# Optimization experiments

Measured on AMD Instinct MI355X. Metric: run time of the kernel, lower is better.

## Reference

```python
import math
import jax, jax.numpy as jnp
import numpy as np

B, N, D, H, NI, NL, NS, MID = 32, 2048, 256, 8, 64, 3, 32, 3


def _ln(x, g, b, eps=1e-5):
    m = jnp.mean(x, axis=-1, keepdims=True)
    v = jnp.mean((x - m) ** 2, axis=-1, keepdims=True)
    return (x - m) * jax.lax.rsqrt(v + eps) * g + b


def _mab(Q, K, mask, Wq, bq, Wk, bk, Wv, bv, Wo, bo, g0, b0, g1, b1):
    # torch's split(dim_split,2)+cat(...,0) == reshape to (B, n, H, dh)
    dh = D // H
    q = (Q @ Wq + bq).reshape(Q.shape[0], Q.shape[1], H, dh)
    k = (K @ Wk + bk).reshape(K.shape[0], K.shape[1], H, dh)
    v = (K @ Wv + bv).reshape(K.shape[0], K.shape[1], H, dh)
    A = jnp.einsum('bqhd,bkhd->bhqk', q, k) / math.sqrt(D)  # note: sqrt(dim_V), faithful
    A = jnp.where(mask[:, None, None, :] == 0, -1e4, A)
    A = jax.nn.softmax(A, axis=-1)
    o = q + jnp.einsum('bhqk,bkhd->bqhd', A, v)
    O = o.reshape(Q.shape[0], Q.shape[1], D)
    O = _ln(O, g0, b0)
    O = O + jax.nn.relu(O @ Wo + bo)
    return _ln(O, g1, b1)


def _forward(x_values, y_target, point_mask, proj_W, proj_b, isab_I,
             isab_Wq, isab_bq, isab_Wk, isab_bk, isab_Wv, isab_bv,
             isab_Wo, isab_bo, isab_g0, isab_b0, isab_g1, isab_b1,
             pma_S, pma_Wq, pma_bq, pma_Wk, pma_bk, pma_Wv, pma_bv,
             pma_Wo, pma_bo, pma_g0, pma_b0, pma_g1, pma_b1):
    # input_dim == max_input_dim, so the zero-padded feature build is a concat
    feats = jnp.concatenate([x_values, y_target[..., None]], axis=-1)  # (B, N, MID+1)
    x = jax.nn.gelu(feats @ proj_W + proj_b, approximate=False)
    ones_mask = jnp.ones((x.shape[0], NI), jnp.float32)
    stk = (isab_Wq, isab_bq, isab_Wk, isab_bk, isab_Wv, isab_bv,
           isab_Wo, isab_bo, isab_g0, isab_b0, isab_g1, isab_b1)
    for l in range(NL):
        I = jnp.broadcast_to(isab_I[l][None], (x.shape[0], NI, D))
        h = _mab(I, x, point_mask, *[a[l, 0] for a in stk])   # mab0: inducing pts attend to X
        x = _mab(x, h, ones_mask, *[a[l, 1] for a in stk])    # mab1: X attends to H (all valid)
    S = jnp.broadcast_to(pma_S[None], (x.shape[0], NS, D))
    return _mab(S, x, point_mask, pma_Wq, pma_bq, pma_Wk, pma_bk, pma_Wv,
                pma_bv, pma_Wo, pma_bo, pma_g0, pma_b0, pma_g1, pma_b1)


def setup_inputs():
    key = jax.random.key(0)
    ks = iter(jax.random.split(key, 40))
    def nrm(shape, s=0.05):
        return jax.random.normal(next(ks), shape, dtype=jnp.float32) * s
    z = lambda shape: jnp.zeros(shape, jnp.float32)
    o = lambda shape: jnp.ones(shape, jnp.float32)
    return {
        'x_values': jax.random.normal(next(ks), (B, N, MID), jnp.float32),
        'y_target': jax.random.normal(next(ks), (B, N), jnp.float32),
        'point_mask': jax.random.randint(next(ks), (B, N), 0, 2).astype(jnp.float32),
        'proj_W': nrm((MID + 1, D)), 'proj_b': z((D,)),
        'isab_I': nrm((NL, NI, D), 0.1),
        'isab_Wq': nrm((NL, 2, D, D)), 'isab_bq': z((NL, 2, D)),
        'isab_Wk': nrm((NL, 2, D, D)), 'isab_bk': z((NL, 2, D)),
        'isab_Wv': nrm((NL, 2, D, D)), 'isab_bv': z((NL, 2, D)),
        'isab_Wo': nrm((NL, 2, D, D)), 'isab_bo': z((NL, 2, D)),
        'isab_g0': o((NL, 2, D)), 'isab_b0': z((NL, 2, D)),
        'isab_g1': o((NL, 2, D)), 'isab_b1': z((NL, 2, D)),
        'pma_S': nrm((NS, D), 0.1),
        'pma_Wq': nrm((D, D)), 'pma_bq': z((D,)),
        'pma_Wk': nrm((D, D)), 'pma_bk': z((D,)),
        'pma_Wv': nrm((D, D)), 'pma_bv': z((D,)),
        'pma_Wo': nrm((D, D)), 'pma_bo': z((D,)),
        'pma_g0': o((D,)), 'pma_b0': z((D,)),
        'pma_g1': o((D,)), 'pma_b1': z((D,)),
    }


def reference(x_values, y_target, point_mask, proj_W, proj_b, isab_I,
              isab_Wq, isab_bq, isab_Wk, isab_bk, isab_Wv, isab_bv,
              isab_Wo, isab_bo, isab_g0, isab_b0, isab_g1, isab_b1,
              pma_S, pma_Wq, pma_bq, pma_Wk, pma_bk, pma_Wv, pma_bv,
              pma_Wo, pma_bo, pma_g0, pma_b0, pma_g1, pma_b1):
    return _forward(x_values, y_target, point_mask, proj_W, proj_b, isab_I,
                    isab_Wq, isab_bq, isab_Wk, isab_bk, isab_Wv, isab_bv,
                    isab_Wo, isab_bo, isab_g0, isab_b0, isab_g1, isab_b1,
                    pma_S, pma_Wq, pma_bq, pma_Wk, pma_bk, pma_Wv, pma_bv,
                    pma_Wo, pma_bo, pma_g0, pma_b0, pma_g1, pma_b1)
```

## Files before the change

kernel.cpp:

```cpp
#include <hip/hip_runtime.h>
#include <hip/hip_bf16.h>


typedef __attribute__((ext_vector_type(8))) short short8;
typedef __attribute__((ext_vector_type(4))) float f32x4;
typedef __attribute__((ext_vector_type(4))) ushort ushort4v;

__device__ __forceinline__ ushort f2bf(float f) {
  uint u = __builtin_bit_cast(uint, f);
  u += 0x7fffu + ((u >> 16) & 1u);
  return (ushort)(u >> 16);
}
__device__ __forceinline__ float bf2f(ushort h) {
  uint u = (uint)h << 16;
  return __builtin_bit_cast(float, u);
}

__global__ __launch_bounds__(256) void prep_weights(
    const float* __restrict__ Wq, const float* __restrict__ Wk,
    const float* __restrict__ Wv, const float* __restrict__ Wo,
    const float* __restrict__ pWq, const float* __restrict__ pWk,
    const float* __restrict__ pWv, const float* __restrict__ pWo,
    ushort* __restrict__ wt)
{
  __shared__ float tile[64][65];
  const int m = blockIdx.y;
  const int t = blockIdx.x;
  const int tr = (t >> 2) * 64;
  const int tc = (t & 3) * 64;
  const float* src;
  if (m < 24) {
    int l = m >> 3, s = (m >> 2) & 1, w = m & 3;
    const float* base = (w == 0) ? Wq : (w == 1) ? Wk : (w == 2) ? Wv : Wo;
    src = base + (size_t)(l * 2 + s) * 65536;
  } else {
    int w = m & 3;
    src = (w == 0) ? pWq : (w == 1) ? pWk : (w == 2) ? pWv : pWo;
  }
  const int tid = threadIdx.x;
  const int cn = tid & 63;
  const int rk = tid >> 6;
#pragma unroll
  for (int j = 0; j < 16; ++j) {
    int kl = rk + j * 4;
    tile[kl][cn] = src[(size_t)(tr + kl) * 256 + tc + cn];
  }
  __syncthreads();
  ushort* dst = wt + (size_t)m * 65536;
#pragma unroll
  for (int j = 0; j < 16; ++j) {
    int nl = rk + j * 4;
    dst[(size_t)(tc + nl) * 256 + tr + cn] = f2bf(tile[cn][nl]);
  }
}

__global__ __launch_bounds__(256) void proj_gelu(
    const float* __restrict__ xv, const float* __restrict__ yt,
    const float* __restrict__ pW, const float* __restrict__ pb,
    ushort* __restrict__ xb)
{
  const int d = threadIdx.x;
  const int row0 = blockIdx.x * 8;
  const float w0 = pW[d], w1 = pW[256 + d], w2 = pW[512 + d], w3 = pW[768 + d];
  const float bz = pb[d];
#pragma unroll
  for (int rr = 0; rr < 8; ++rr) {
    int row = row0 + rr;
    float f0 = xv[(size_t)row * 3 + 0];
    float f1 = xv[(size_t)row * 3 + 1];
    float f2 = xv[(size_t)row * 3 + 2];
    float f3 = yt[row];
    float a = bz + f0 * w0 + f1 * w1 + f2 * w2 + f3 * w3;
    float g = 0.5f * a * (1.f + erff(a * 0.70710678118654752f));
    xb[(size_t)row * 256 + d] = f2bf(g);
  }
}

__global__ __launch_bounds__(256) void gemm_q(
    const float* __restrict__ iI, const float* __restrict__ pS,
    const ushort* __restrict__ wt, const float* __restrict__ ibq,
    const float* __restrict__ pbq, ushort* __restrict__ q_all)
{
  const int bq = blockIdx.x;
  const float* A; const ushort* Wt; const float* bias; ushort* out; int M;
  if (bq < 3) { A = iI + bq * 16384; Wt = wt + (size_t)(bq * 8) * 65536; bias = ibq + bq * 512; out = q_all + bq * 16384; M = 64; }
  else        { A = pS; Wt = wt + (size_t)24 * 65536; bias = pbq; out = q_all + 49152; M = 32; }
  const int tid = threadIdx.x;
  const int wave = tid >> 6, lane = tid & 63;
  const int l15 = lane & 15, l4 = lane >> 4, koff = l4 * 8;
  f32x4 acc[4][4];
#pragma unroll
  for (int i = 0; i < 4; ++i)
#pragma unroll
    for (int j = 0; j < 4; ++j) acc[i][j] = (f32x4)0.f;
#pragma unroll
  for (int ks = 0; ks < 8; ++ks) {
    short8 af[4];
#pragma unroll
    for (int mf = 0; mf < 4; ++mf) {
      if (mf * 16 < M) {
        const float* ap = A + (size_t)(mf * 16 + l15) * 256 + ks * 32 + koff;
        float4 f0 = *(const float4*)ap;
        float4 f1 = *(const float4*)(ap + 4);
        short8 sv;
        sv[0] = (short)f2bf(f0.x); sv[1] = (short)f2bf(f0.y);
        sv[2] = (short)f2bf(f0.z); sv[3] = (short)f2bf(f0.w);
        sv[4] = (short)f2bf(f1.x); sv[5] = (short)f2bf(f1.y);
        sv[6] = (short)f2bf(f1.z); sv[7] = (short)f2bf(f1.w);
        af[mf] = sv;
      } else af[mf] = (short8)0;
    }
#pragma unroll
    for (int nf = 0; nf < 4; ++nf) {
      short8 bf = *(const short8*)(Wt + (size_t)(wave * 64 + nf * 16 + l15) * 256 + ks * 32 + koff);
#pragma unroll
      for (int mf = 0; mf < 4; ++mf)
        acc[mf][nf] = __builtin_amdgcn_mfma_f32_16x16x32_bf16(af[mf], bf, acc[mf][nf], 0, 0, 0);
    }
  }
#pragma unroll
  for (int mf = 0; mf < 4; ++mf) {
    if (mf * 16 >= M) continue;
#pragma unroll
    for (int nf = 0; nf < 4; ++nf) {
      int col = wave * 64 + nf * 16 + l15;
      float bcol = bias[col];
#pragma unroll
      for (int r = 0; r < 4; ++r)
        out[(size_t)(mf * 16 + l4 * 4 + r) * 256 + col] = f2bf(acc[mf][nf][r] + bcol);
    }
  }
}

template <int EPI, bool OUTF32, int COLS>
__global__ __launch_bounds__(COLS * 2, (COLS == 128) ? 4 : 2) void gemm_bp(
    const ushort* __restrict__ A,
    const ushort* __restrict__ Wt0, const ushort* __restrict__ Wt1, const ushort* __restrict__ Wt2,
    const float* __restrict__ b0, const float* __restrict__ b1, const float* __restrict__ b2,
    void* __restrict__ o0, void* __restrict__ o1, void* __restrict__ o2,
    const float* __restrict__ lng, const float* __restrict__ lnb,
    int ny, int nyz)
{
  constexpr int WC = COLS / 64;
  constexpr int PS = COLS * 64;
  constexpr int ROWB = COLS * 2;
  __shared__ __align__(16) char Bs[4 * PS];
  __shared__ float redbuf[(EPI == 3) ? 1280 : 4];
  const int bid = blockIdx.x;
  const int rest = bid >> 3;
  const int yz = rest % nyz;
  const int bx = ((rest / nyz) << 3) | (bid & 7);
  const int y = yz % ny;
  const int z = yz / ny;
  const ushort* Wt = (z == 0) ? Wt0 : ((z == 1) ? Wt1 : Wt2);
  const float* bias = (z == 0) ? b0 : ((z == 1) ? b1 : b2);
  void* outp = (z == 0) ? o0 : ((z == 1) ? o1 : o2);
  const int pcol = y * COLS;

  const int tid = threadIdx.x;
  const int wave = tid >> 6, lane = tid & 63;
  const int wc = wave % WC, wr = wave / WC;
  const int l15 = lane & 15, l4 = lane >> 4;
  const int row0 = bx * 128;
  const int sn = tid >> 1, sseg = tid & 1;

  f32x4 acc[4][4];
#pragma unroll
  for (int i = 0; i < 4; ++i)
#pragma unroll
    for (int j = 0; j < 4; ++j) acc[i][j] = (f32x4)0.f;

#pragma unroll
  for (int half = 0; half < 2; ++half) {
    if (half) __syncthreads();
    {
      const ushort* src = Wt + (size_t)(pcol + sn) * 256 + half * 128 + sseg * 64;
#pragma unroll
      for (int c = 0; c < 8; ++c) {
        uint4 w = *(const uint4*)(src + c * 8);
        int plane = sseg * 2 + (c >> 2);
        char* dst = Bs + plane * PS + sn * 64 + (((c & 3) * 16) ^ (((sn >> 1) & 3) << 4));
        *(uint4*)dst = w;
      }
    }
    __syncthreads();
#pragma unroll
    for (int ks = 0; ks < 4; ++ks) {
      short8 af[4];
#pragma unroll
      for (int mfa = 0; mfa < 4; ++mfa)
        af[mfa] = *(const short8*)(A + (size_t)(row0 + wr * 64 + mfa * 16 + l15) * 256 + half * 128 + ks * 32 + l4 * 8);
#pragma unroll
      for (int nfb = 0; nfb < 4; ++nfb) {
        int n = wc * 64 + nfb * 16 + l15;
        short8 bf = *(const short8*)(Bs + ks * PS + n * 64 + ((l4 * 16) ^ (((n >> 1) & 3) << 4)));
#pragma unroll
        for (int mfa = 0; mfa < 4; ++mfa)
          acc[mfa][nfb] = __builtin_amdgcn_mfma_f32_16x16x32_bf16(bf, af[mfa], acc[mfa][nfb], 0, 0, 0);
      }
    }
  }

  if constexpr (EPI == 0) {
    __syncthreads();
#pragma unroll
    for (int nfb = 0; nfb < 4; ++nfb) {
      f32x4 bv = *(const f32x4*)(bias + pcol + wc * 64 + nfb * 16 + l4 * 4);
      int colb = wc * 128 + nfb * 32 + l4 * 8;
#pragma unroll
      for (int mfa = 0; mfa < 4; ++mfa) {
        int row = wr * 64 + mfa * 16 + l15;
        ushort4v pk;
#pragma unroll
        for (int i = 0; i < 4; ++i) pk[i] = f2bf(acc[mfa][nfb][i] + bv[i]);
        *(ushort4v*)(Bs + row * ROWB + (colb ^ ((row & 7) << 4))) = pk;
      }
    }
    __syncthreads();
    const int srow = tid >> 2, seg = tid & 3;
#pragma unroll
    for (int rr = 0; rr < 2; ++rr) {
      int row = srow + rr * 64;
      int x = (row & 7) << 4;
      ushort* gdst = (ushort*)outp + (size_t)(row0 + row) * 256 + pcol;
#pragma unroll
      for (int it = 0; it < 4; ++it) {
        int colb = seg * 16 + it * 64;
        uint4 v = *(const uint4*)(Bs + row * ROWB + (colb ^ x));
        *(uint4*)(gdst + colb / 2) = v;
      }
    }
  } else {
    float* red1 = redbuf;
    float* red2 = redbuf + 512;
    float* mv_ = redbuf + 1024;
    float* rv_ = redbuf + 1152;
    float s1[4] = {0.f, 0.f, 0.f, 0.f}, s2[4] = {0.f, 0.f, 0.f, 0.f};
#pragma unroll
    for (int nfb = 0; nfb < 4; ++nfb) {
      int col0 = wc * 64 + nfb * 16 + l4 * 4;
      f32x4 bv = *(const f32x4*)(bias + col0);
#pragma unroll
      for (int mfa = 0; mfa < 4; ++mfa) {
        size_t row = (size_t)row0 + wr * 64 + mfa * 16 + l15;
        ushort4v rz = *(const ushort4v*)(A + row * 256 + col0);
#pragma unroll
        for (int i = 0; i < 4; ++i) {
          float zz = bf2f(rz[i]) + fmaxf(acc[mfa][nfb][i] + bv[i], 0.f);
          acc[mfa][nfb][i] = zz;
          s1[mfa] += zz;
          s2[mfa] += zz * zz;
        }
      }
    }
#pragma unroll
    for (int mfa = 0; mfa < 4; ++mfa) {
      s1[mfa] += __shfl_xor(s1[mfa], 16); s1[mfa] += __shfl_xor(s1[mfa], 32);
      s2[mfa] += __shfl_xor(s2[mfa], 16); s2[mfa] += __shfl_xor(s2[mfa], 32);
    }
    if (l4 == 0) {
#pragma unroll
      for (int mfa = 0; mfa < 4; ++mfa) {
        red1[wc * 128 + wr * 64 + mfa * 16 + l15] = s1[mfa];
        red2[wc * 128 + wr * 64 + mfa * 16 + l15] = s2[mfa];
      }
    }
    __syncthreads();
    if (tid < 128) {
      float m1 = red1[tid] + red1[128 + tid] + red1[256 + tid] + red1[384 + tid];
      float m2 = red2[tid] + red2[128 + tid] + red2[256 + tid] + red2[384 + tid];
      float mean = m1 * 0.00390625f;
      float var = m2 * 0.00390625f - mean * mean;
      mv_[tid] = mean;
      rv_[tid] = rsqrtf(var + 1e-5f);
    }
    __syncthreads();
#pragma unroll
    for (int nfb = 0; nfb < 4; ++nfb) {
      int col0 = wc * 64 + nfb * 16 + l4 * 4;
      f32x4 gg = *(const f32x4*)(lng + col0);
      f32x4 bb = *(const f32x4*)(lnb + col0);
      int colb = col0 * 2;
#pragma unroll
      for (int mfa = 0; mfa < 4; ++mfa) {
        int lr = wr * 64 + mfa * 16 + l15;
        float mean = mv_[lr], rs = rv_[lr];
        if constexpr (OUTF32) {
          f32x4 w;
#pragma unroll
          for (int i = 0; i < 4; ++i) w[i] = (acc[mfa][nfb][i] - mean) * rs * gg[i] + bb[i];
          *(f32x4*)((float*)outp + ((size_t)row0 + lr) * 256 + col0) = w;
        } else {
          ushort4v pk;
#pragma unroll
          for (int i = 0; i < 4; ++i) pk[i] = f2bf((acc[mfa][nfb][i] - mean) * rs * gg[i] + bb[i]);
          *(ushort4v*)(Bs + lr * ROWB + (colb ^ ((lr & 7) << 4))) = pk;
        }
      }
    }
    if constexpr (!OUTF32) {
      __syncthreads();
      const int srow = tid >> 2, seg = tid & 3;
      int x = (srow & 7) << 4;
      ushort* gdst = (ushort*)outp + (size_t)(row0 + srow) * 256;
#pragma unroll
      for (int it = 0; it < 8; ++it) {
        int colb = seg * 16 + it * 64;
        uint4 v = *(const uint4*)(Bs + srow * ROWB + (colb ^ x));
        *(uint4*)(gdst + colb / 2) = v;
      }
    }
  }
}

template <int MF>
__global__ __launch_bounds__(512) void attn_big(
    const ushort* __restrict__ qb, const ushort* __restrict__ kb,
    const ushort* __restrict__ vb, const float* __restrict__ mask,
    ushort* __restrict__ O)
{
  __shared__ __align__(16) ushort Ps[8][64][72];
  __shared__ __align__(16) ushort Vt[8][32][72];
  const int h = blockIdx.x, b = blockIdx.y;
  const int tid = threadIdx.x;
  const int w = tid >> 6, lane = tid & 63;
  const int l15 = lane & 15, l4 = lane >> 4;
  const int koff = l4 * 8;
  const int kvbase = b * 2048;

  short8 qf[MF];
#pragma unroll
  for (int mf = 0; mf < MF; ++mf)
    qf[mf] = *(const short8*)(qb + (size_t)(mf * 16 + l15) * 256 + h * 32 + koff);

  f32x4 Oa[MF][2];
  float Mr[MF][4], Lr[MF][4];
#pragma unroll
  for (int mf = 0; mf < MF; ++mf) {
    Oa[mf][0] = (f32x4)0.f; Oa[mf][1] = (f32x4)0.f;
#pragma unroll
    for (int r = 0; r < 4; ++r) { Mr[mf][r] = -1e30f; Lr[mf][r] = 0.f; }
  }

  for (int c = 0; c < 4; ++c) {
    const int kc = w * 256 + c * 64;
    f32x4 S[MF][4];
#pragma unroll
    for (int nf = 0; nf < 4; ++nf) {
      short8 kf = *(const short8*)(kb + (size_t)(kvbase + kc + nf * 16 + l15) * 256 + h * 32 + koff);
#pragma unroll
      for (int mf = 0; mf < MF; ++mf)
        S[mf][nf] = __builtin_amdgcn_mfma_f32_16x16x32_bf16(qf[mf], kf, (f32x4)0.f, 0, 0, 0);
    }
    float mv[4];
#pragma unroll
    for (int nf = 0; nf < 4; ++nf)
      mv[nf] = mask[(size_t)b * 2048 + kc + nf * 16 + l15];
#pragma unroll
    for (int mf = 0; mf < MF; ++mf)
#pragma unroll
      for (int nf = 0; nf < 4; ++nf)
#pragma unroll
        for (int r = 0; r < 4; ++r) {
          float s = S[mf][nf][r] * 0.0625f;
          S[mf][nf][r] = (mv[nf] != 0.f) ? s : -1e4f;
        }
#pragma unroll
    for (int mf = 0; mf < MF; ++mf)
#pragma unroll
      for (int r = 0; r < 4; ++r) {
        float pm = fmaxf(fmaxf(S[mf][0][r], S[mf][1][r]), fmaxf(S[mf][2][r], S[mf][3][r]));
        pm = fmaxf(pm, __shfl_xor(pm, 1));
        pm = fmaxf(pm, __shfl_xor(pm, 2));
        pm = fmaxf(pm, __shfl_xor(pm, 4));
        pm = fmaxf(pm, __shfl_xor(pm, 8));
        float Mnew = fmaxf(Mr[mf][r], pm);
        float corr = __expf(Mr[mf][r] - Mnew);
        Mr[mf][r] = Mnew;
        float rs = 0.f;
#pragma unroll
        for (int nf = 0; nf < 4; ++nf) {
          float p = __expf(S[mf][nf][r] - Mnew);
          S[mf][nf][r] = p;
          rs += p;
        }
        rs += __shfl_xor(rs, 1);
        rs += __shfl_xor(rs, 2);
        rs += __shfl_xor(rs, 4);
        rs += __shfl_xor(rs, 8);
        Lr[mf][r] = Lr[mf][r] * corr + rs;
        Oa[mf][0][r] *= corr;
        Oa[mf][1][r] *= corr;
      }
#pragma unroll
    for (int dblk = 0; dblk < 4; ++dblk) {
      short8 vv = *(const short8*)(vb + (size_t)(kvbase + kc + lane) * 256 + h * 32 + dblk * 8);
#pragma unroll
      for (int j = 0; j < 8; ++j) Vt[w][dblk * 8 + j][lane] = (ushort)vv[j];
    }
#pragma unroll
    for (int mf = 0; mf < MF; ++mf)
#pragma unroll
      for (int nf = 0; nf < 4; ++nf)
#pragma unroll
        for (int r = 0; r < 4; ++r)
          Ps[w][mf * 16 + l4 * 4 + r][nf * 16 + l15] = f2bf(S[mf][nf][r]);
#pragma unroll
    for (int ks = 0; ks < 2; ++ks) {
      short8 pf[MF];
#pragma unroll
      for (int mf = 0; mf < MF; ++mf)
        pf[mf] = *(const short8*)&Ps[w][mf * 16 + l15][ks * 32 + koff];
#pragma unroll
      for (int nf2 = 0; nf2 < 2; ++nf2) {
        short8 vf = *(const short8*)&Vt[w][nf2 * 16 + l15][ks * 32 + koff];
#pragma unroll
        for (int mf = 0; mf < MF; ++mf)
          Oa[mf][nf2] = __builtin_amdgcn_mfma_f32_16x16x32_bf16(pf[mf], vf, Oa[mf][nf2], 0, 0, 0);
      }
    }
  }

  __syncthreads();
  float* Mw = (float*)&Ps[0][0][0];
  float* Lw = Mw + 512;
  float* Ow = Lw + 512;
#pragma unroll
  for (int mf = 0; mf < MF; ++mf)
#pragma unroll
    for (int r = 0; r < 4; ++r) {
      int row = mf * 16 + l4 * 4 + r;
      if (l15 == 0) { Mw[w * 64 + row] = Mr[mf][r]; Lw[w * 64 + row] = Lr[mf][r]; }
#pragma unroll
      for (int nf2 = 0; nf2 < 2; ++nf2)
        Ow[(w * 64 + row) * 33 + nf2 * 16 + l15] = Oa[mf][nf2][r];
    }
  __syncthreads();
  const int NQ = MF * 16;
  int row = tid >> 3, dg = tid & 7;
  if (row < NQ) {
    float mm = -1e30f;
#pragma unroll
    for (int s = 0; s < 8; ++s) mm = fmaxf(mm, Mw[s * 64 + row]);
    float den = 0.f, es[8];
#pragma unroll
    for (int s = 0; s < 8; ++s) {
      es[s] = __expf(Mw[s * 64 + row] - mm);
      den += Lw[s * 64 + row] * es[s];
    }
    float invden = 1.f / den;
    ushort4v pk;
#pragma unroll
    for (int i = 0; i < 4; ++i) {
      int d = dg * 4 + i;
      float num = 0.f;
#pragma unroll
      for (int s = 0; s < 8; ++s) num += Ow[(s * 64 + row) * 33 + d] * es[s];
      float qv = bf2f(qb[(size_t)row * 256 + h * 32 + d]);
      pk[i] = f2bf(qv + num * invden);
    }
    *(ushort4v*)(O + (size_t)(b * NQ + row) * 256 + h * 32 + dg * 4) = pk;
  }
}

__global__ __launch_bounds__(512, 4) void mab1_fused(
    const ushort* __restrict__ xb, const ushort* __restrict__ wq,
    const float* __restrict__ bq,
    const ushort* __restrict__ kb, const ushort* __restrict__ vb,
    const ushort* __restrict__ wo, const float* __restrict__ bo,
    const float* __restrict__ g0, const float* __restrict__ b0v,
    const float* __restrict__ g1, const float* __restrict__ b1v,
    ushort* __restrict__ outb)
{
  __shared__ __align__(16) ushort Qs[8][64][40];
  __shared__ __align__(16) ushort Psh[8][16][40];
  __shared__ __align__(16) ushort Vth[8][32][40];
  __shared__ float red1[8][64], red2[8][64], mv_[64], rv_[64];
  ushort* o_s = &Qs[0][0][0];
  constexpr int OS = 264;

  const int qt = blockIdx.x, b = blockIdx.y;
  const int tid = threadIdx.x;
  const int w = tid >> 6, lane = tid & 63;
  const int l15 = lane & 15, l4 = lane >> 4;
  const int koff = l4 * 8;
  const size_t row0 = (size_t)b * 2048 + qt * 64;
  const int kvbase = b * 64;
  const int h = w;

  short8 kf[4];
#pragma unroll
  for (int nf = 0; nf < 4; ++nf)
    kf[nf] = *(const short8*)(kb + (size_t)(kvbase + nf * 16 + l15) * 256 + h * 32 + koff);
  const int key = lane & 31, dh2 = lane >> 5;
  short8 vvB0, vvB1;
  {
    const ushort* vsrcA = vb + (size_t)(kvbase + key) * 256 + h * 32 + dh2 * 16;
    const ushort* vsrcB = vb + (size_t)(kvbase + 32 + key) * 256 + h * 32 + dh2 * 16;
    short8 vvA0 = *(const short8*)vsrcA;
    short8 vvA1 = *(const short8*)(vsrcA + 8);
    vvB0 = *(const short8*)vsrcB;
    vvB1 = *(const short8*)(vsrcB + 8);
#pragma unroll
    for (int j = 0; j < 8; ++j) Vth[w][dh2 * 16 + j][key] = (ushort)vvA0[j];
#pragma unroll
    for (int j = 0; j < 8; ++j) Vth[w][dh2 * 16 + 8 + j][key] = (ushort)vvA1[j];
  }

  {
    f32x4 qa[4][2];
#pragma unroll
    for (int i = 0; i < 4; ++i) { qa[i][0] = (f32x4)0.f; qa[i][1] = (f32x4)0.f; }
#pragma unroll
    for (int ks = 0; ks < 8; ++ks) {
      short8 af[4];
#pragma unroll
      for (int mfa = 0; mfa < 4; ++mfa)
        af[mfa] = *(const short8*)(xb + (row0 + mfa * 16 + l15) * 256 + ks * 32 + koff);
#pragma unroll
      for (int nfb = 0; nfb < 2; ++nfb) {
        int n = w * 32 + nfb * 16 + l15;
        short8 bf = *(const short8*)(wq + (size_t)n * 256 + ks * 32 + koff);
#pragma unroll
        for (int mfa = 0; mfa < 4; ++mfa)
          qa[mfa][nfb] = __builtin_amdgcn_mfma_f32_16x16x32_bf16(bf, af[mfa], qa[mfa][nfb], 0, 0, 0);
      }
    }
#pragma unroll
    for (int nfb = 0; nfb < 2; ++nfb) {
      f32x4 bv = *(const f32x4*)(bq + w * 32 + nfb * 16 + l4 * 4);
#pragma unroll
      for (int mfa = 0; mfa < 4; ++mfa) {
        ushort4v pk;
#pragma unroll
        for (int i = 0; i < 4; ++i) pk[i] = f2bf(qa[mfa][nfb][i] + bv[i]);
        *(ushort4v*)&Qs[w][mfa * 16 + l15][nfb * 16 + l4 * 4] = pk;
      }
    }
  }

  short8 qf[4];
#pragma unroll
  for (int mf = 0; mf < 4; ++mf)
    qf[mf] = *(const short8*)&Qs[w][mf * 16 + l15][koff];

  f32x4 S[4][4];
#pragma unroll
  for (int nf = 0; nf < 4; ++nf) {
#pragma unroll
    for (int mf = 0; mf < 4; ++mf)
      S[mf][nf] = __builtin_amdgcn_mfma_f32_16x16x32_bf16(qf[mf], kf[nf], (f32x4)0.f, 0, 0, 0);
  }
  float Lr[4][4];
#pragma unroll
  for (int mf = 0; mf < 4; ++mf)
#pragma unroll
    for (int r = 0; r < 4; ++r) {
      float pm = fmaxf(fmaxf(S[mf][0][r], S[mf][1][r]), fmaxf(S[mf][2][r], S[mf][3][r])) * 0.0625f;
      pm = fmaxf(pm, __shfl_xor(pm, 1));
      pm = fmaxf(pm, __shfl_xor(pm, 2));
      pm = fmaxf(pm, __shfl_xor(pm, 4));
      pm = fmaxf(pm, __shfl_xor(pm, 8));
      float rs = 0.f;
#pragma unroll
      for (int nf = 0; nf < 4; ++nf) {
        float p = __expf(S[mf][nf][r] * 0.0625f - pm);
        S[mf][nf][r] = p;
        rs += p;
      }
      rs += __shfl_xor(rs, 1);
      rs += __shfl_xor(rs, 2);
      rs += __shfl_xor(rs, 4);
      rs += __shfl_xor(rs, 8);
      Lr[mf][r] = rs;
    }

  f32x4 Oa[4][2];
#pragma unroll
  for (int mf = 0; mf < 4; ++mf) { Oa[mf][0] = (f32x4)0.f; Oa[mf][1] = (f32x4)0.f; }
#pragma unroll
  for (int mf = 0; mf < 4; ++mf) {
#pragma unroll
    for (int nf = 0; nf < 2; ++nf)
#pragma unroll
      for (int r = 0; r < 4; ++r)
        Psh[w][l4 * 4 + r][nf * 16 + l15] = f2bf(S[mf][nf][r]);
    short8 pf = *(const short8*)&Psh[w][l15][koff];
#pragma unroll
    for (int nf2 = 0; nf2 < 2; ++nf2) {
      short8 vf = *(const short8*)&Vth[w][nf2 * 16 + l15][koff];
      Oa[mf][nf2] = __builtin_amdgcn_mfma_f32_16x16x32_bf16(pf, vf, Oa[mf][nf2], 0, 0, 0);
    }
  }
#pragma unroll
  for (int j = 0; j < 8; ++j) Vth[w][dh2 * 16 + j][key] = (ushort)vvB0[j];
#pragma unroll
  for (int j = 0; j < 8; ++j) Vth[w][dh2 * 16 + 8 + j][key] = (ushort)vvB1[j];
#pragma unroll
  for (int mf = 0; mf < 4; ++mf) {
#pragma unroll
    for (int nf = 0; nf < 2; ++nf)
#pragma unroll
      for (int r = 0; r < 4; ++r)
        Psh[w][l4 * 4 + r][nf * 16 + l15] = f2bf(S[mf][nf + 2][r]);
    short8 pf = *(const short8*)&Psh[w][l15][koff];
#pragma unroll
    for (int nf2 = 0; nf2 < 2; ++nf2) {
      short8 vf = *(const short8*)&Vth[w][nf2 * 16 + l15][koff];
      Oa[mf][nf2] = __builtin_amdgcn_mfma_f32_16x16x32_bf16(pf, vf, Oa[mf][nf2], 0, 0, 0);
    }
  }

  {
    float s1[4][4], s2[4][4];
#pragma unroll
    for (int mf = 0; mf < 4; ++mf)
#pragma unroll
      for (int r = 0; r < 4; ++r) {
        float invL = 1.f / Lr[mf][r];
        s1[mf][r] = 0.f; s2[mf][r] = 0.f;
#pragma unroll
        for (int nf2 = 0; nf2 < 2; ++nf2) {
          float qv = bf2f(Qs[w][mf * 16 + l4 * 4 + r][nf2 * 16 + l15]);
          float z = qv + Oa[mf][nf2][r] * invL;
          Oa[mf][nf2][r] = z;
          s1[mf][r] += z;
          s2[mf][r] += z * z;
        }
#pragma unroll
        for (int off = 1; off < 16; off <<= 1) {
          s1[mf][r] += __shfl_xor(s1[mf][r], off);
          s2[mf][r] += __shfl_xor(s2[mf][r], off);
        }
        if (l15 == 0) {
          int row = mf * 16 + l4 * 4 + r;
          red1[w][row] = s1[mf][r];
          red2[w][row] = s2[mf][r];
        }
      }
  }
  __syncthreads();
  if (tid < 64) {
    float m1 = 0.f, m2 = 0.f;
#pragma unroll
    for (int s = 0; s < 8; ++s) { m1 += red1[s][tid]; m2 += red2[s][tid]; }
    float mean = m1 * 0.00390625f;
    float var = m2 * 0.00390625f - mean * mean;
    mv_[tid] = mean;
    rv_[tid] = rsqrtf(var + 1e-5f);
  }
  __syncthreads();
#pragma unroll
  for (int nf2 = 0; nf2 < 2; ++nf2) {
    int col = h * 32 + nf2 * 16 + l15;
    float gc = g0[col], bc = b0v[col];
#pragma unroll
    for (int mf = 0; mf < 4; ++mf)
#pragma unroll
      for (int r = 0; r < 4; ++r) {
        int row = mf * 16 + l4 * 4 + r;
        float v = (Oa[mf][nf2][r] - mv_[row]) * rv_[row] * gc + bc;
        o_s[row * OS + col] = f2bf(v);
      }
  }
  __syncthreads();

  f32x4 oa[4][2];
#pragma unroll
  for (int i = 0; i < 4; ++i) { oa[i][0] = (f32x4)0.f; oa[i][1] = (f32x4)0.f; }
#pragma unroll
  for (int ks = 0; ks < 8; ++ks) {
    short8 af[4];
#pragma unroll
    for (int mfa = 0; mfa < 4; ++mfa)
      af[mfa] = *(const short8*)&o_s[(mfa * 16 + l15) * OS + ks * 32 + koff];
#pragma unroll
    for (int nfb = 0; nfb < 2; ++nfb) {
      int n = w * 32 + nfb * 16 + l15;
      short8 bf = *(const short8*)(wo + (size_t)n * 256 + ks * 32 + koff);
#pragma unroll
      for (int mfa = 0; mfa < 4; ++mfa)
        oa[mfa][nfb] = __builtin_amdgcn_mfma_f32_16x16x32_bf16(bf, af[mfa], oa[mfa][nfb], 0, 0, 0);
    }
  }
  float t1[4] = {0.f, 0.f, 0.f, 0.f}, t2[4] = {0.f, 0.f, 0.f, 0.f};
#pragma unroll
  for (int nfb = 0; nfb < 2; ++nfb) {
    int col0 = w * 32 + nfb * 16 + l4 * 4;
    f32x4 bv = *(const f32x4*)(bo + col0);
#pragma unroll
    for (int mfa = 0; mfa < 4; ++mfa) {
      int row = mfa * 16 + l15;
      ushort4v rz = *(const ushort4v*)&o_s[row * OS + col0];
#pragma unroll
      for (int i = 0; i < 4; ++i) {
        float zz = bf2f(rz[i]) + fmaxf(oa[mfa][nfb][i] + bv[i], 0.f);
        oa[mfa][nfb][i] = zz;
        t1[mfa] += zz;
        t2[mfa] += zz * zz;
      }
    }
  }
#pragma unroll
  for (int mfa = 0; mfa < 4; ++mfa) {
    t1[mfa] += __shfl_xor(t1[mfa], 16); t1[mfa] += __shfl_xor(t1[mfa], 32);
    t2[mfa] += __shfl_xor(t2[mfa], 16); t2[mfa] += __shfl_xor(t2[mfa], 32);
  }
  if (l4 == 0) {
#pragma unroll
    for (int mfa = 0; mfa < 4; ++mfa) {
      red1[w][mfa * 16 + l15] = t1[mfa];
      red2[w][mfa * 16 + l15] = t2[mfa];
    }
  }
  __syncthreads();
  if (tid < 64) {
    float m1 = 0.f, m2 = 0.f;
#pragma unroll
    for (int s = 0; s < 8; ++s) { m1 += red1[s][tid]; m2 += red2[s][tid]; }
    float mean = m1 * 0.00390625f;
    float var = m2 * 0.00390625f - mean * mean;
    mv_[tid] = mean;
    rv_[tid] = rsqrtf(var + 1e-5f);
  }
  __syncthreads();
#pragma unroll
  for (int nfb = 0; nfb < 2; ++nfb) {
    int col0 = w * 32 + nfb * 16 + l4 * 4;
    f32x4 gg = *(const f32x4*)(g1 + col0);
    f32x4 bb = *(const f32x4*)(b1v + col0);
#pragma unroll
    for (int mfa = 0; mfa < 4; ++mfa) {
      int row = mfa * 16 + l15;
      ushort4v pk;
#pragma unroll
      for (int i = 0; i < 4; ++i)
        pk[i] = f2bf((oa[mfa][nfb][i] - mv_[row]) * rv_[row] * gg[i] + bb[i]);
      *(ushort4v*)&o_s[row * OS + col0] = pk;
    }
  }
  __syncthreads();
  {
    const int r_ = tid >> 3, sg = tid & 7;
    ushort* gdst = outb + (row0 + r_) * 256 + sg * 32;
    const ushort* src = &o_s[r_ * OS + sg * 32];
#pragma unroll
    for (int it = 0; it < 4; ++it) {
      uint4 v = *(const uint4*)(src + it * 8);
      *(uint4*)(gdst + it * 8) = v;
    }
  }
}

__global__ __launch_bounds__(256) void ln4(
    const ushort* __restrict__ in, ushort* __restrict__ out,
    const float* __restrict__ g, const float* __restrict__ bb)
{
  const int w = threadIdx.x >> 6, lane = threadIdx.x & 63;
  const size_t row = (size_t)blockIdx.x * 4 + w;
  ushort4v u = *(const ushort4v*)(in + row * 256 + lane * 4);
  float v[4];
#pragma unroll
  for (int i = 0; i < 4; ++i) v[i] = bf2f(u[i]);
  float s1 = v[0] + v[1] + v[2] + v[3];
  float s2 = v[0] * v[0] + v[1] * v[1] + v[2] * v[2] + v[3] * v[3];
#pragma unroll
  for (int off = 1; off < 64; off <<= 1) {
    s1 += __shfl_xor(s1, off);
    s2 += __shfl_xor(s2, off);
  }
  float mean = s1 * 0.00390625f;
  float var = s2 * 0.00390625f - mean * mean;
  float rs = rsqrtf(var + 1e-5f);
  f32x4 gg = *(const f32x4*)(g + lane * 4);
  f32x4 bv = *(const f32x4*)(bb + lane * 4);
  ushort4v p;
#pragma unroll
  for (int i = 0; i < 4; ++i) p[i] = f2bf((v[i] - mean) * rs * gg[i] + bv[i]);
  *(ushort4v*)(out + row * 256 + lane * 4) = p;
}

extern "C" void kernel_launch(void* const* d_in, const int* in_sizes, int n_in,
                              void* d_out, int out_size, void* d_ws, size_t ws_size,
                              hipStream_t stream) {
  const float* xv = (const float*)d_in[0];
  const float* yt = (const float*)d_in[1];
  const float* pmask = (const float*)d_in[2];
  const float* prW = (const float*)d_in[3];
  const float* prb = (const float*)d_in[4];
  const float* iI = (const float*)d_in[5];
  const float* iWq = (const float*)d_in[6];
  const float* ibq = (const float*)d_in[7];
  const float* iWk = (const float*)d_in[8];
  const float* ibk = (const float*)d_in[9];
  const float* iWv = (const float*)d_in[10];
  const float* ibv = (const float*)d_in[11];
  const float* iWo = (const float*)d_in[12];
  const float* ibo = (const float*)d_in[13];
  const float* ig0 = (const float*)d_in[14];
  const float* ib0 = (const float*)d_in[15];
  const float* ig1 = (const float*)d_in[16];
  const float* ib1 = (const float*)d_in[17];
  const float* pS = (const float*)d_in[18];
  const float* pWq = (const float*)d_in[19];
  const float* pbq = (const float*)d_in[20];
  const float* pWk = (const float*)d_in[21];
  const float* pbk = (const float*)d_in[22];
  const float* pWv = (const float*)d_in[23];
  const float* pbv = (const float*)d_in[24];
  const float* pWo = (const float*)d_in[25];
  const float* pbo = (const float*)d_in[26];
  const float* pg0 = (const float*)d_in[27];
  const float* pb0 = (const float*)d_in[28];
  const float* pg1 = (const float*)d_in[29];
  const float* pb1 = (const float*)d_in[30];

  char* ws = (char*)d_ws;
  if (ws_size < 172621824u) return;
  ushort* xb = (ushort*)(ws + 0);
  ushort* ob = (ushort*)(ws + 33554432);
  ushort* hb = (ushort*)(ws + 67108864);
  ushort* kbw = (ushort*)(ws + 101711872);
  ushort* vbw = (ushort*)(ws + 135266304);
  ushort* wt = (ushort*)(ws + 168820736);
  ushort* q_all = (ushort*)(ws + 172490752);

  prep_weights<<<dim3(16, 28), 256, 0, stream>>>(iWq, iWk, iWv, iWo, pWq, pWk, pWv, pWo, wt);
  proj_gelu<<<8192, 256, 0, stream>>>(xv, yt, prW, prb, xb);
  gemm_q<<<4, 256, 0, stream>>>(iI, pS, wt, ibq, pbq, q_all);

  for (int l = 0; l < 3; ++l) {
    const int s0 = l * 2, s1 = l * 2 + 1;
    const ushort* wk = wt + (size_t)(l * 8 + 1) * 65536;
    const ushort* wv = wt + (size_t)(l * 8 + 2) * 65536;
    const ushort* wo0 = wt + (size_t)(l * 8 + 3) * 65536;
    const ushort* wq1 = wt + (size_t)(l * 8 + 4) * 65536;
    const ushort* wk1 = wt + (size_t)(l * 8 + 5) * 65536;
    const ushort* wv1 = wt + (size_t)(l * 8 + 6) * 65536;
    const ushort* wo1 = wt + (size_t)(l * 8 + 7) * 65536;
    gemm_bp<0, false, 128><<<2048, 256, 0, stream>>>(
        xb, wk, wv, wv, ibk + s0 * 256, ibv + s0 * 256, ibv + s0 * 256,
        kbw, vbw, vbw, nullptr, nullptr, 2, 4);
    attn_big<4><<<dim3(8, 32), 512, 0, stream>>>(q_all + l * 16384, kbw, vbw, pmask, ob);
    ln4<<<512, 256, 0, stream>>>(ob, ob, ig0 + s0 * 256, ib0 + s0 * 256);
    gemm_bp<3, false, 256><<<16, 512, 0, stream>>>(
        ob, wo0, wo0, wo0, ibo + s0 * 256, ibo + s0 * 256, ibo + s0 * 256,
        hb, hb, hb, ig1 + s0 * 256, ib1 + s0 * 256, 1, 1);
    gemm_bp<0, false, 128><<<64, 256, 0, stream>>>(
        hb, wk1, wv1, wv1, ibk + s1 * 256, ibv + s1 * 256, ibv + s1 * 256,
        kbw, vbw, vbw, nullptr, nullptr, 2, 4);
    mab1_fused<<<dim3(32, 32), 512, 0, stream>>>(
        xb, wq1, ibq + s1 * 256, kbw, vbw, wo1, ibo + s1 * 256,
        ig0 + s1 * 256, ib0 + s1 * 256, ig1 + s1 * 256, ib1 + s1 * 256, xb);
  }
  gemm_bp<0, false, 128><<<2048, 256, 0, stream>>>(
      xb, wt + (size_t)25 * 65536, wt + (size_t)26 * 65536, wt + (size_t)26 * 65536,
      pbk, pbv, pbv, kbw, vbw, vbw, nullptr, nullptr, 2, 4);
  attn_big<2><<<dim3(8, 32), 512, 0, stream>>>(q_all + 49152, kbw, vbw, pmask, ob);
  ln4<<<256, 256, 0, stream>>>(ob, ob, pg0, pb0);
  gemm_bp<3, true, 256><<<8, 512, 0, stream>>>(
      ob, wt + (size_t)27 * 65536, wt + (size_t)27 * 65536, wt + (size_t)27 * 65536,
      pbo, pbo, pbo, d_out, d_out, d_out, pg1, pb1, 1, 1);
}
```

Baseline: 799.5 us.

## Fuse K/V projection of X into the inducing-point attention kernel

The separate gemm_bp launch that projected all 65536 points to K and V is removed. The attention kernel, now with a (batch, head) grid, computes each head's 32-column slice of K and V on the fly from the bf16 X tile with MFMAs and stages the results in shared memory. This removes the global write and re-read of K/V, which are large (B*N*D in bf16, written then read back), and one kernel launch per layer. In exchange each block rereads the full 256-wide X rows once per head, so X traffic goes up eightfold (mostly from L2). It also adds projection compute inside the attention kernel, plus extra shared memory and registers.

```diff
diff --git a/kernel.cpp b/kernel.cpp
--- a/kernel.cpp
+++ b/kernel.cpp
@@ -314,14 +314,16 @@
 }
 
 template <int MF>
-__global__ __launch_bounds__(512) void attn_big(
-    const ushort* __restrict__ qb, const ushort* __restrict__ kb,
-    const ushort* __restrict__ vb, const float* __restrict__ mask,
-    ushort* __restrict__ O)
+__global__ __launch_bounds__(512) void attn_fused(
+    const ushort* __restrict__ qb, const ushort* __restrict__ xbuf,
+    const ushort* __restrict__ wk, const float* __restrict__ bk,
+    const ushort* __restrict__ wv, const float* __restrict__ bv,
+    const float* __restrict__ mask, ushort* __restrict__ O)
 {
   __shared__ __align__(16) ushort Ps[8][64][72];
   __shared__ __align__(16) ushort Vt[8][32][72];
-  const int h = blockIdx.x, b = blockIdx.y;
+  __shared__ __align__(16) ushort Kc[8][64][40];
+  const int b = blockIdx.x, h = blockIdx.y;
   const int tid = threadIdx.x;
   const int w = tid >> 6, lane = tid & 63;
   const int l15 = lane & 15, l4 = lane >> 4;
@@ -333,6 +335,13 @@
   for (int mf = 0; mf < MF; ++mf)
     qf[mf] = *(const short8*)(qb + (size_t)(mf * 16 + l15) * 256 + h * 32 + koff);
 
+  f32x4 bkv[2], bvv[2];
+#pragma unroll
+  for (int nfb = 0; nfb < 2; ++nfb) {
+    bkv[nfb] = *(const f32x4*)(bk + h * 32 + nfb * 16 + l4 * 4);
+    bvv[nfb] = *(const f32x4*)(bv + h * 32 + nfb * 16 + l4 * 4);
+  }
+
   f32x4 Oa[MF][2];
   float Mr[MF][4], Lr[MF][4];
 #pragma unroll
@@ -344,10 +353,51 @@
 
   for (int c = 0; c < 4; ++c) {
     const int kc = w * 256 + c * 64;
+    f32x4 ak[4][2], av[4][2];
+#pragma unroll
+    for (int i = 0; i < 4; ++i) {
+      ak[i][0] = (f32x4)0.f; ak[i][1] = (f32x4)0.f;
+      av[i][0] = (f32x4)0.f; av[i][1] = (f32x4)0.f;
+    }
+#pragma unroll
+    for (int ks = 0; ks < 8; ++ks) {
+      short8 af[4];
+#pragma unroll
+      for (int mfa = 0; mfa < 4; ++mfa)
+        af[mfa] = *(const short8*)(xbuf + (size_t)(kvbase + kc + mfa * 16 + l15) * 256 + ks * 32 + koff);
+#pragma unroll
+      for (int nfb = 0; nfb < 2; ++nfb) {
+        int n = h * 32 + nfb * 16 + l15;
+        short8 wkf = *(const short8*)(wk + (size_t)n * 256 + ks * 32 + koff);
+        short8 wvf = *(const short8*)(wv + (size_t)n * 256 + ks * 32 + koff);
+#pragma unroll
+        for (int mfa = 0; mfa < 4; ++mfa) {
+          ak[mfa][nfb] = __builtin_amdgcn_mfma_f32_16x16x32_bf16(wkf, af[mfa], ak[mfa][nfb], 0, 0, 0);
+          av[mfa][nfb] = __builtin_amdgcn_mfma_f32_16x16x32_bf16(wvf, af[mfa], av[mfa][nfb], 0, 0, 0);
+        }
+      }
+    }
+#pragma unroll
+    for (int nfb = 0; nfb < 2; ++nfb)
+#pragma unroll
+      for (int mfa = 0; mfa < 4; ++mfa) {
+        ushort4v pk;
+#pragma unroll
+        for (int i = 0; i < 4; ++i) pk[i] = f2bf(ak[mfa][nfb][i] + bkv[nfb][i]);
+        *(ushort4v*)&Kc[w][mfa * 16 + l15][nfb * 16 + l4 * 4] = pk;
+      }
+#pragma unroll
+    for (int nfb = 0; nfb < 2; ++nfb)
+#pragma unroll
+      for (int mfa = 0; mfa < 4; ++mfa)
+#pragma unroll
+        for (int i = 0; i < 4; ++i)
+          Vt[w][nfb * 16 + l4 * 4 + i][mfa * 16 + l15] = f2bf(av[mfa][nfb][i] + bvv[nfb][i]);
+
     f32x4 S[MF][4];
 #pragma unroll
     for (int nf = 0; nf < 4; ++nf) {
-      short8 kf = *(const short8*)(kb + (size_t)(kvbase + kc + nf * 16 + l15) * 256 + h * 32 + koff);
+      short8 kf = *(const short8*)&Kc[w][nf * 16 + l15][koff];
 #pragma unroll
       for (int mf = 0; mf < MF; ++mf)
         S[mf][nf] = __builtin_amdgcn_mfma_f32_16x16x32_bf16(qf[mf], kf, (f32x4)0.f, 0, 0, 0);
@@ -392,12 +442,6 @@
         Oa[mf][0][r] *= corr;
         Oa[mf][1][r] *= corr;
       }
-#pragma unroll
-    for (int dblk = 0; dblk < 4; ++dblk) {
-      short8 vv = *(const short8*)(vb + (size_t)(kvbase + kc + lane) * 256 + h * 32 + dblk * 8);
-#pragma unroll
-      for (int j = 0; j < 8; ++j) Vt[w][dblk * 8 + j][lane] = (ushort)vv[j];
-    }
 #pragma unroll
     for (int mf = 0; mf < MF; ++mf)
 #pragma unroll
@@ -528,12 +572,12 @@
     }
 #pragma unroll
     for (int nfb = 0; nfb < 2; ++nfb) {
-      f32x4 bv = *(const f32x4*)(bq + w * 32 + nfb * 16 + l4 * 4);
+      f32x4 bvq = *(const f32x4*)(bq + w * 32 + nfb * 16 + l4 * 4);
 #pragma unroll
       for (int mfa = 0; mfa < 4; ++mfa) {
         ushort4v pk;
 #pragma unroll
-        for (int i = 0; i < 4; ++i) pk[i] = f2bf(qa[mfa][nfb][i] + bv[i]);
+        for (int i = 0; i < 4; ++i) pk[i] = f2bf(qa[mfa][nfb][i] + bvq[i]);
         *(ushort4v*)&Qs[w][mfa * 16 + l15][nfb * 16 + l4 * 4] = pk;
       }
     }
@@ -687,14 +731,14 @@
 #pragma unroll
   for (int nfb = 0; nfb < 2; ++nfb) {
     int col0 = w * 32 + nfb * 16 + l4 * 4;
-    f32x4 bv = *(const f32x4*)(bo + col0);
+    f32x4 bvo = *(const f32x4*)(bo + col0);
 #pragma unroll
     for (int mfa = 0; mfa < 4; ++mfa) {
       int row = mfa * 16 + l15;
       ushort4v rz = *(const ushort4v*)&o_s[row * OS + col0];
 #pragma unroll
       for (int i = 0; i < 4; ++i) {
-        float zz = bf2f(rz[i]) + fmaxf(oa[mfa][nfb][i] + bv[i], 0.f);
+        float zz = bf2f(rz[i]) + fmaxf(oa[mfa][nfb][i] + bvo[i], 0.f);
         oa[mfa][nfb][i] = zz;
         t1[mfa] += zz;
         t2[mfa] += zz * zz;
@@ -838,10 +882,8 @@
     const ushort* wk1 = wt + (size_t)(l * 8 + 5) * 65536;
     const ushort* wv1 = wt + (size_t)(l * 8 + 6) * 65536;
     const ushort* wo1 = wt + (size_t)(l * 8 + 7) * 65536;
-    gemm_bp<0, false, 128><<<2048, 256, 0, stream>>>(
-        xb, wk, wv, wv, ibk + s0 * 256, ibv + s0 * 256, ibv + s0 * 256,
-        kbw, vbw, vbw, nullptr, nullptr, 2, 4);
-    attn_big<4><<<dim3(8, 32), 512, 0, stream>>>(q_all + l * 16384, kbw, vbw, pmask, ob);
+    attn_fused<4><<<dim3(32, 8), 512, 0, stream>>>(
+        q_all + l * 16384, xb, wk, ibk + s0 * 256, wv, ibv + s0 * 256, pmask, ob);
     ln4<<<512, 256, 0, stream>>>(ob, ob, ig0 + s0 * 256, ib0 + s0 * 256);
     gemm_bp<3, false, 256><<<16, 512, 0, stream>>>(
         ob, wo0, wo0, wo0, ibo + s0 * 256, ibo + s0 * 256, ibo + s0 * 256,
@@ -853,10 +895,8 @@
         xb, wq1, ibq + s1 * 256, kbw, vbw, wo1, ibo + s1 * 256,
         ig0 + s1 * 256, ib0 + s1 * 256, ig1 + s1 * 256, ib1 + s1 * 256, xb);
   }
-  gemm_bp<0, false, 128><<<2048, 256, 0, stream>>>(
-      xb, wt + (size_t)25 * 65536, wt + (size_t)26 * 65536, wt + (size_t)26 * 65536,
-      pbk, pbv, pbv, kbw, vbw, vbw, nullptr, nullptr, 2, 4);
-  attn_big<2><<<dim3(8, 32), 512, 0, stream>>>(q_all + 49152, kbw, vbw, pmask, ob);
+  attn_fused<2><<<dim3(32, 8), 512, 0, stream>>>(
+      q_all + 49152, xb, wt + (size_t)25 * 65536, pbk, wt + (size_t)26 * 65536, pbv, pmask, ob);
   ln4<<<256, 256, 0, stream>>>(ob, ob, pg0, pb0);
   gemm_bp<3, true, 256><<<8, 512, 0, stream>>>(
       ob, wt + (size_t)27 * 65536, wt + (size_t)27 * 65536, wt + (size_t)27 * 65536,
```

Result: no change. 793.0 us (-0.8%).
